# Kernel tuning notes

Measured on AMD Instinct MI355X. Metric: run time of the kernel, lower is better.

## Reference

```python
import jax, jax.numpy as jnp
import numpy as np

N_EMBED = 384
N_HEAD = 6
HEAD_DIM = N_EMBED // N_HEAD


def setup_inputs() -> dict:
    key = jax.random.key(0)
    k1, k2, k3 = jax.random.split(key, 3)
    B, T = 128, 256
    x = jax.random.normal(k1, (B, T, N_EMBED), dtype=jnp.float32)
    # nn.Linear(N_EMBED, 3*N_EMBED, bias=False): weight [3*N_EMBED, N_EMBED],
    # applied as x @ W.T -> store transposed [N_EMBED, 3*N_EMBED]
    W_qkv = jax.random.normal(k2, (N_EMBED, 3 * N_EMBED), dtype=jnp.float32) * (N_EMBED ** -0.5)
    W_proj = jax.random.normal(k3, (N_EMBED, N_EMBED), dtype=jnp.float32) * (N_EMBED ** -0.5)
    return {"x": x, "W_qkv": W_qkv, "W_proj": W_proj}


def reference(x, W_qkv, W_proj):
    B, T, C = x.shape
    qkv = jnp.einsum('btc,cd->btd', x, W_qkv)  # [B,T,3C]
    q, k, v = jnp.split(qkv, 3, axis=-1)
    # [B, H, T, Dh]
    q = q.reshape(B, T, N_HEAD, HEAD_DIM).transpose(0, 2, 1, 3)
    k = k.reshape(B, T, N_HEAD, HEAD_DIM).transpose(0, 2, 1, 3)
    v = v.reshape(B, T, N_HEAD, HEAD_DIM).transpose(0, 2, 1, 3)
    scale = HEAD_DIM ** -0.5
    wei = jnp.einsum('bhqd,bhkd->bhqk', q, k) * scale  # [B,H,T,T]
    causal = jnp.tril(jnp.ones((T, T), dtype=bool))
    wei = jnp.where(causal[None, None, :, :], wei, -jnp.inf)
    wei = jax.nn.softmax(wei, axis=-1)
    # dropout layers are identity in eval mode
    out = jnp.einsum('bhqk,bhkd->bhqd', wei, v)  # [B,H,T,Dh]
    out = out.transpose(0, 2, 1, 3).reshape(B, T, C)
    out = jnp.einsum('btc,cd->btd', out, W_proj)
    return out
```

## Files before the change

### kernel.cpp

```cpp
#include <hip/hip_runtime.h>
#include <hip/hip_bf16.h>

typedef __attribute__((ext_vector_type(8))) short short8;
typedef __attribute__((ext_vector_type(4))) float f32x4;
typedef __attribute__((ext_vector_type(4))) unsigned short ush4;

typedef const __attribute__((address_space(1))) void* gas_p;
typedef __attribute__((address_space(3))) void* las_p;
#define GLOAD_LDS16(g, l) __builtin_amdgcn_global_load_lds((gas_p)(const void*)(g), (las_p)(void*)(l), 16, 0, 0)

__device__ __forceinline__ unsigned short f2bf(float f) {
    union { float f; unsigned int u; } v; v.f = f;
    unsigned int r = v.u + 0x7FFFu + ((v.u >> 16) & 1u);
    return (unsigned short)(r >> 16);
}
__device__ __forceinline__ unsigned pk2(float a, float b) {
    return (unsigned)f2bf(a) | ((unsigned)f2bf(b) << 16);
}

__global__ __launch_bounds__(256) void cast_wt_kernel(
    const float* __restrict__ W, unsigned short* __restrict__ Wt, int K, int N)
{
    int idx = blockIdx.x * 256 + threadIdx.x;
    if (idx >= N * K) return;
    int n = idx / K, k = idx - n * K;
    Wt[idx] = f2bf(W[(size_t)k * N + n]);
}

__global__ __launch_bounds__(256, 2) void gemm_qkv_kernel(
    const float* __restrict__ x,
    const unsigned short* __restrict__ Bt,
    unsigned short* __restrict__ qkb,
    unsigned short* __restrict__ vtb)
{
    const int K = 384;
    __shared__ __align__(16) unsigned short Sh[2 * 128 * 64];
    unsigned short* As = Sh;
    unsigned short* Bs = Sh + 128 * 64;
    const int tid = threadIdx.x;
    const int lane = tid & 63, wv = tid >> 6;
    const int c = lane & 15, g = lane >> 4;
    const int wm = (wv >> 1) * 64, wn = (wv & 1) * 64;

    const int id = blockIdx.x, xcd = id & 7, kk = id >> 3;
    const long m0 = (long)(xcd * 32 + kk / 9) * 128;
    const long n0 = (long)(kk % 9) * 128;

    f32x4 acc[4][4] = {};
    const int xr = (c & 7) << 4;

    for (int kt = 0; kt < K; kt += 64) {
        #pragma unroll
        for (int i = 0; i < 4; ++i) {
            int ch = i * 256 + tid;
            int row = ch >> 3, cc = ch & 7;
            GLOAD_LDS16(&Bt[(n0 + row) * (size_t)K + kt + (cc ^ (row & 7)) * 8],
                        &Bs[(i * 256 + wv * 64) * 8]);
        }
        #pragma unroll
        for (int i = 0; i < 4; ++i) {
            int ch = i * 256 + tid;
            int row = ch >> 3, cc = ch & 7;
            const float* ga = &x[(m0 + row) * (size_t)K + kt + (cc ^ (row & 7)) * 8];
            float4 a = *(const float4*)ga;
            float4 b = *(const float4*)(ga + 4);
            uint4 w;
            w.x = pk2(a.x, a.y); w.y = pk2(a.z, a.w);
            w.z = pk2(b.x, b.y); w.w = pk2(b.z, b.w);
            *(uint4*)&As[ch * 8] = w;
        }
        __syncthreads();
        #pragma unroll
        for (int ks = 0; ks < 2; ++ks) {
            short8 af[4], bf_[4];
            #pragma unroll
            for (int i = 0; i < 4; ++i)
                af[i] = *(const short8*)((char*)As +
                    (((wm + i * 16 + c) * 128 + (ks * 32 + g * 8) * 2) ^ xr));
            #pragma unroll
            for (int i = 0; i < 4; ++i)
                bf_[i] = *(const short8*)((char*)Bs +
                    (((wn + i * 16 + c) * 128 + (ks * 32 + g * 8) * 2) ^ xr));
            #pragma unroll
            for (int mi = 0; mi < 4; ++mi)
                #pragma unroll
                for (int ni = 0; ni < 4; ++ni)
                    acc[mi][ni] = __builtin_amdgcn_mfma_f32_16x16x32_bf16(
                        af[mi], bf_[ni], acc[mi][ni], 0, 0, 0);
        }
        __syncthreads();
    }

    if (n0 < 768) {
        #pragma unroll
        for (int mi = 0; mi < 4; ++mi)
            #pragma unroll
            for (int ni = 0; ni < 4; ++ni)
                #pragma unroll
                for (int r = 0; r < 4; ++r) {
                    long m = m0 + wm + mi * 16 + g * 4 + r;
                    long n = n0 + wn + ni * 16 + c;
                    qkb[m * 768 + n] = f2bf(acc[mi][ni][r]);
                }
    } else {
        char* wbase = (char*)Sh + wv * 8192;
        #pragma unroll
        for (int ni = 0; ni < 4; ++ni)
            #pragma unroll
            for (int mi = 0; mi < 4; ++mi)
                #pragma unroll
                for (int r = 0; r < 4; ++r) {
                    int d = ni * 16 + c, t = mi * 16 + g * 4 + r;
                    int byte = (d * 128 + t * 2) ^ ((d & 7) << 4);
                    *(unsigned short*)(wbase + byte) = f2bf(acc[mi][ni][r]);
                }
        __asm__ __volatile__("" ::: "memory");
        int h = (int)((n0 + wn - 768) >> 6);
        long b = (m0 + wm) >> 8;
        int t0 = (int)((m0 + wm) & 255);
        long bh = b * 6 + h;
        #pragma unroll
        for (int it = 0; it < 8; ++it) {
            int d = it * 8 + (lane >> 3), ck = lane & 7;
            short8 v = *(const short8*)(wbase + ((d * 128 + ck * 16) ^ ((d & 7) << 4)));
            *(short8*)&vtb[(bh * 64 + d) * 256 + t0 + ck * 8] = v;
        }
    }
}

__global__ __launch_bounds__(256, 2) void gemm_proj_kernel(
    const unsigned short* __restrict__ A, const unsigned short* __restrict__ Bt,
    float* __restrict__ C, int M, int N, int K)
{
    __shared__ __align__(16) unsigned short As[128 * 64];
    __shared__ __align__(16) unsigned short Bs[128 * 64];
    const int tid = threadIdx.x;
    const int lane = tid & 63, wv = tid >> 6;
    const int c = lane & 15, g = lane >> 4;
    const int wm = (wv >> 1) * 64, wn = (wv & 1) * 64;

    const int mpx = (M >> 7) >> 3;
    const int id = blockIdx.x, xcd = id & 7, kk = id >> 3;
    const long m0 = (long)(xcd * mpx + (kk % mpx)) * 128;
    const long n0 = (long)(kk / mpx) * 128;

    f32x4 acc[4][4] = {};
    const int xr = (c & 7) << 4;

    for (int kt = 0; kt < K; kt += 64) {
        #pragma unroll
        for (int i = 0; i < 4; ++i) {
            int ch = i * 256 + wv * 64 + lane;
            int row = ch >> 3, cc = ch & 7;
            int sc = (cc ^ (row & 7)) * 8;
            GLOAD_LDS16(&A[(m0 + row) * (size_t)K + kt + sc],
                        &As[(i * 256 + wv * 64) * 8]);
            GLOAD_LDS16(&Bt[(n0 + row) * (size_t)K + kt + sc],
                        &Bs[(i * 256 + wv * 64) * 8]);
        }
        __syncthreads();
        #pragma unroll
        for (int ks = 0; ks < 2; ++ks) {
            short8 af[4], bf_[4];
            #pragma unroll
            for (int i = 0; i < 4; ++i)
                af[i] = *(const short8*)((char*)As +
                    (((wm + i * 16 + c) * 128 + (ks * 32 + g * 8) * 2) ^ xr));
            #pragma unroll
            for (int i = 0; i < 4; ++i)
                bf_[i] = *(const short8*)((char*)Bs +
                    (((wn + i * 16 + c) * 128 + (ks * 32 + g * 8) * 2) ^ xr));
            #pragma unroll
            for (int mi = 0; mi < 4; ++mi)
                #pragma unroll
                for (int ni = 0; ni < 4; ++ni)
                    acc[mi][ni] = __builtin_amdgcn_mfma_f32_16x16x32_bf16(
                        af[mi], bf_[ni], acc[mi][ni], 0, 0, 0);
        }
        __syncthreads();
    }

    #pragma unroll
    for (int mi = 0; mi < 4; ++mi)
        #pragma unroll
        for (int ni = 0; ni < 4; ++ni)
            #pragma unroll
            for (int r = 0; r < 4; ++r) {
                long m = m0 + wm + mi * 16 + g * 4 + r;
                long n = n0 + wn + ni * 16 + c;
                C[m * N + n] = acc[mi][ni][r];
            }
}

__global__ __launch_bounds__(256, 3) void attn_kernel(
    const unsigned short* __restrict__ qk,
    const unsigned short* __restrict__ vt,
    unsigned short* __restrict__ outp)
{
    const int bh = blockIdx.x;
    const int b = bh / 6, h = bh - b * 6;
    const int tid = threadIdx.x;
    const int lane = tid & 63, wv = tid >> 6;
    const int c = lane & 15, g = lane >> 4;

    __shared__ unsigned short Ks[256 * 64];
    __shared__ unsigned short Pl[4][16 * 64];

    #pragma unroll
    for (int it = 0; it < 8; ++it) {
        int ch = it * 256 + tid;
        int row = ch >> 3, col = (ch & 7) * 8;
        int db = (row * 128 + col * 2) ^ ((row & 7) << 4);
        *(short8*)((char*)Ks + db) =
            *(const short8*)&qk[(size_t)(b * 256 + row) * 768 + 384 + h * 64 + col];
    }
    __syncthreads();

    char* plw = (char*)Pl[wv];

    for (int t = 0; t < 2; ++t) {
        const int p = t ? 7 - wv : wv;
        const int jlast = p >> 1;
        const int modd = (p & 1) * 32;
        const int qt0 = p * 32;

        short8 aq[2][2];
        #pragma unroll
        for (int mi = 0; mi < 2; ++mi)
            #pragma unroll
            for (int ks = 0; ks < 2; ++ks)
                aq[mi][ks] = *(const short8*)&qk[
                    (size_t)(b * 256 + qt0 + mi * 16 + c) * 768 + h * 64 + ks * 32 + g * 8];

        f32x4 o[2][4] = {};
        float mrun[2] = {-1e30f, -1e30f}, lrun[2] = {0.f, 0.f};

        for (int j = 0; j <= jlast; ++j) {
            short8 bv[4][2];
            #pragma unroll
            for (int nd = 0; nd < 4; ++nd)
                #pragma unroll
                for (int ks = 0; ks < 2; ++ks)
                    bv[nd][ks] = *(const short8*)&vt[
                        ((size_t)bh * 64 + nd * 16 + c) * 256 + j * 64 + ks * 32 + g * 8];

            short8 bk[4][2];
            #pragma unroll
            for (int ni = 0; ni < 4; ++ni)
                #pragma unroll
                for (int ks = 0; ks < 2; ++ks) {
                    int key = j * 64 + ni * 16 + c;
                    bk[ni][ks] = *(const short8*)((char*)Ks +
                        ((key * 128 + (ks * 32 + g * 8) * 2) ^ ((key & 7) << 4)));
                }

            #pragma unroll
            for (int mi = 0; mi < 2; ++mi) {
                float pv[4][4];
                #pragma unroll
                for (int ni = 0; ni < 4; ++ni) {
                    f32x4 z = {0.f, 0.f, 0.f, 0.f};
                    z = __builtin_amdgcn_mfma_f32_16x16x32_bf16(bk[ni][0], aq[mi][0], z, 0, 0, 0);
                    z = __builtin_amdgcn_mfma_f32_16x16x32_bf16(bk[ni][1], aq[mi][1], z, 0, 0, 0);
                    #pragma unroll
                    for (int r = 0; r < 4; ++r) {
                        float v = z[r] * 0.125f;
                        if (j == jlast) {
                            int kloc = ni * 16 + g * 4 + r;
                            int qloc = mi * 16 + c + modd;
                            if (kloc > qloc) v = -1e30f;
                        }
                        pv[ni][r] = v;
                    }
                }
                float m01 = fmaxf(fmaxf(pv[0][0], pv[0][1]), fmaxf(pv[0][2], pv[0][3]));
                float m11 = fmaxf(fmaxf(pv[1][0], pv[1][1]), fmaxf(pv[1][2], pv[1][3]));
                float m21 = fmaxf(fmaxf(pv[2][0], pv[2][1]), fmaxf(pv[2][2], pv[2][3]));
                float m31 = fmaxf(fmaxf(pv[3][0], pv[3][1]), fmaxf(pv[3][2], pv[3][3]));
                float m1 = fmaxf(fmaxf(m01, m11), fmaxf(m21, m31));
                m1 = fmaxf(m1, __shfl_xor(m1, 16));
                m1 = fmaxf(m1, __shfl_xor(m1, 32));
                float mold = mrun[mi];
                float mnew = fmaxf(mold, m1);
                float fac = __expf(mold - mnew);
                float ssum = 0.f;
                #pragma unroll
                for (int ni = 0; ni < 4; ++ni)
                    #pragma unroll
                    for (int r = 0; r < 4; ++r) {
                        float pp = __expf(pv[ni][r] - mnew);
                        pv[ni][r] = pp;
                        ssum += pp;
                    }
                ssum += __shfl_xor(ssum, 16);
                ssum += __shfl_xor(ssum, 32);
                lrun[mi] = lrun[mi] * fac + ssum;
                mrun[mi] = mnew;
                #pragma unroll
                for (int nd = 0; nd < 4; ++nd)
                    #pragma unroll
                    for (int r = 0; r < 4; ++r) o[mi][nd][r] *= fac;

                __asm__ __volatile__("" ::: "memory");
                #pragma unroll
                for (int ni = 0; ni < 4; ++ni) {
                    uint2 w;
                    w.x = pk2(pv[ni][0], pv[ni][1]);
                    w.y = pk2(pv[ni][2], pv[ni][3]);
                    *(uint2*)(plw + ((c * 128 + ni * 32 + g * 8) ^ ((c & 7) << 4))) = w;
                }
                __asm__ __volatile__("" ::: "memory");

                short8 ap[2];
                #pragma unroll
                for (int ks = 0; ks < 2; ++ks)
                    ap[ks] = *(const short8*)(plw +
                        ((c * 128 + ks * 64 + g * 16) ^ ((c & 7) << 4)));

                #pragma unroll
                for (int nd = 0; nd < 4; ++nd) {
                    o[mi][nd] = __builtin_amdgcn_mfma_f32_16x16x32_bf16(bv[nd][0], ap[0], o[mi][nd], 0, 0, 0);
                    o[mi][nd] = __builtin_amdgcn_mfma_f32_16x16x32_bf16(bv[nd][1], ap[1], o[mi][nd], 0, 0, 0);
                }
                __asm__ __volatile__("" ::: "memory");
            }
        }

        #pragma unroll
        for (int mi = 0; mi < 2; ++mi) {
            float inv = 1.0f / lrun[mi];
            #pragma unroll
            for (int nd = 0; nd < 4; ++nd) {
                ush4 w;
                #pragma unroll
                for (int r = 0; r < 4; ++r) w[r] = f2bf(o[mi][nd][r] * inv);
                *(ush4*)&outp[((size_t)b * 256 + qt0 + mi * 16 + c) * 384 + h * 64 + nd * 16 + g * 4] = w;
            }
        }
    }
}

extern "C" void kernel_launch(void* const* d_in, const int* in_sizes, int n_in,
                              void* d_out, int out_size, void* d_ws, size_t ws_size,
                              hipStream_t stream) {
    const float* x     = (const float*)d_in[0];
    const float* Wqkv  = (const float*)d_in[1];
    const float* Wproj = (const float*)d_in[2];

    char* ws = (char*)d_ws;
    unsigned short* wqkvt  = (unsigned short*)(ws);
    unsigned short* wprojt = (unsigned short*)(ws + 884736);
    unsigned short* qkb    = (unsigned short*)(ws + 1179648);
    unsigned short* vtb    = (unsigned short*)(ws + 51511296);
    unsigned short* attnb  = (unsigned short*)(ws + 76677120);

    cast_wt_kernel<<<1728, 256, 0, stream>>>(Wqkv, wqkvt, 384, 1152);
    cast_wt_kernel<<<576, 256, 0, stream>>>(Wproj, wprojt, 384, 384);

    gemm_qkv_kernel<<<2304, 256, 0, stream>>>(x, wqkvt, qkb, vtb);
    attn_kernel<<<768, 256, 0, stream>>>(qkb, vtb, attnb);
    gemm_proj_kernel<<<768, 256, 0, stream>>>(attnb, wprojt, (float*)d_out, 32768, 384, 384);
}
```

Baseline: 125.1 us.

## Load fp32 x directly into LDS and convert on read; merge weight casts

The QKV GEMM now streams fp32 x into LDS with async global_load_lds and converts to bf16 during fragment reads using v_cvt_pk_bf16_f32, replacing the register-staged load, convert and LDS store. The goal is to overlap the A-tile load with the B load and remove VGPR staging. The cost is doubled A-tile LDS footprint (48KB total), which may limit occupancy. The two weight-cast launches are merged into one kernel, and the proj GEMM tile ordering puts the N tiles innermost so neighbouring blocks share A rows.

```diff
diff --git a/kernel.cpp b/kernel.cpp
--- a/kernel.cpp
+++ b/kernel.cpp
@@ -18,13 +18,20 @@
     return (unsigned)f2bf(a) | ((unsigned)f2bf(b) << 16);
 }
 
-__global__ __launch_bounds__(256) void cast_wt_kernel(
-    const float* __restrict__ W, unsigned short* __restrict__ Wt, int K, int N)
+__global__ __launch_bounds__(256) void cast_w_kernel(
+    const float* __restrict__ Wqkv, const float* __restrict__ Wproj,
+    unsigned short* __restrict__ wqkvt, unsigned short* __restrict__ wprojt)
 {
-    int idx = blockIdx.x * 256 + threadIdx.x;
-    if (idx >= N * K) return;
-    int n = idx / K, k = idx - n * K;
-    Wt[idx] = f2bf(W[(size_t)k * N + n]);
+    const int bid = blockIdx.x;
+    if (bid < 1728) {
+        int idx = bid * 256 + threadIdx.x;
+        int n = idx / 384, k = idx - n * 384;
+        wqkvt[idx] = f2bf(Wqkv[(size_t)k * 1152 + n]);
+    } else {
+        int idx = (bid - 1728) * 256 + threadIdx.x;
+        int n = idx / 384, k = idx - n * 384;
+        wprojt[idx] = f2bf(Wproj[(size_t)k * 384 + n]);
+    }
 }
 
 __global__ __launch_bounds__(256, 2) void gemm_qkv_kernel(
@@ -34,9 +41,9 @@
     unsigned short* __restrict__ vtb)
 {
     const int K = 384;
-    __shared__ __align__(16) unsigned short Sh[2 * 128 * 64];
-    unsigned short* As = Sh;
-    unsigned short* Bs = Sh + 128 * 64;
+    __shared__ __align__(16) char Sh[48 * 1024];
+    char* Af = Sh;
+    char* Bs = Sh + 32768;
     const int tid = threadIdx.x;
     const int lane = tid & 63, wv = tid >> 6;
     const int c = lane & 15, g = lane >> 4;
@@ -51,35 +58,41 @@
 
     for (int kt = 0; kt < K; kt += 64) {
         #pragma unroll
+        for (int i = 0; i < 8; ++i) {
+            int ch = i * 256 + wv * 64 + lane;
+            int row = ch >> 4, cc = ch & 15;
+            GLOAD_LDS16(&x[(m0 + row) * (size_t)K + kt + ((cc ^ (row & 7)) << 2)],
+                        Af + (i * 256 + wv * 64) * 16);
+        }
+        #pragma unroll
         for (int i = 0; i < 4; ++i) {
-            int ch = i * 256 + tid;
+            int ch = i * 256 + wv * 64 + lane;
             int row = ch >> 3, cc = ch & 7;
-            GLOAD_LDS16(&Bt[(n0 + row) * (size_t)K + kt + (cc ^ (row & 7)) * 8],
-                        &Bs[(i * 256 + wv * 64) * 8]);
-        }
-        #pragma unroll
-        for (int i = 0; i < 4; ++i) {
-            int ch = i * 256 + tid;
-            int row = ch >> 3, cc = ch & 7;
-            const float* ga = &x[(m0 + row) * (size_t)K + kt + (cc ^ (row & 7)) * 8];
-            float4 a = *(const float4*)ga;
-            float4 b = *(const float4*)(ga + 4);
-            uint4 w;
-            w.x = pk2(a.x, a.y); w.y = pk2(a.z, a.w);
-            w.z = pk2(b.x, b.y); w.w = pk2(b.z, b.w);
-            *(uint4*)&As[ch * 8] = w;
+            GLOAD_LDS16(&Bt[(n0 + row) * (size_t)K + kt + ((cc ^ (row & 7)) << 3)],
+                        Bs + (i * 256 + wv * 64) * 16);
         }
         __syncthreads();
         #pragma unroll
         for (int ks = 0; ks < 2; ++ks) {
             short8 af[4], bf_[4];
             #pragma unroll
+            for (int i = 0; i < 4; ++i) {
+                int row = wm + i * 16 + c;
+                int ch0 = ks * 8 + g * 2;
+                f32x4 lo = *(const f32x4*)(Af + row * 256 + ((ch0 ^ (c & 7)) << 4));
+                f32x4 hi = *(const f32x4*)(Af + row * 256 + (((ch0 + 1) ^ (c & 7)) << 4));
+                unsigned r0, r1, r2, r3;
+                asm("v_cvt_pk_bf16_f32 %0, %1, %2" : "=v"(r0) : "v"(lo[0]), "v"(lo[1]));
+                asm("v_cvt_pk_bf16_f32 %0, %1, %2" : "=v"(r1) : "v"(lo[2]), "v"(lo[3]));
+                asm("v_cvt_pk_bf16_f32 %0, %1, %2" : "=v"(r2) : "v"(hi[0]), "v"(hi[1]));
+                asm("v_cvt_pk_bf16_f32 %0, %1, %2" : "=v"(r3) : "v"(hi[2]), "v"(hi[3]));
+                union { uint4 u4; short8 s8; } cv;
+                cv.u4.x = r0; cv.u4.y = r1; cv.u4.z = r2; cv.u4.w = r3;
+                af[i] = cv.s8;
+            }
+            #pragma unroll
             for (int i = 0; i < 4; ++i)
-                af[i] = *(const short8*)((char*)As +
-                    (((wm + i * 16 + c) * 128 + (ks * 32 + g * 8) * 2) ^ xr));
-            #pragma unroll
-            for (int i = 0; i < 4; ++i)
-                bf_[i] = *(const short8*)((char*)Bs +
+                bf_[i] = *(const short8*)(Bs +
                     (((wn + i * 16 + c) * 128 + (ks * 32 + g * 8) * 2) ^ xr));
             #pragma unroll
             for (int mi = 0; mi < 4; ++mi)
@@ -103,7 +116,7 @@
                     qkb[m * 768 + n] = f2bf(acc[mi][ni][r]);
                 }
     } else {
-        char* wbase = (char*)Sh + wv * 8192;
+        char* wbase = Af + wv * 8192;
         #pragma unroll
         for (int ni = 0; ni < 4; ++ni)
             #pragma unroll
@@ -128,6 +141,7 @@
     }
 }
 
+template<int NP>
 __global__ __launch_bounds__(256, 2) void gemm_proj_kernel(
     const unsigned short* __restrict__ A, const unsigned short* __restrict__ Bt,
     float* __restrict__ C, int M, int N, int K)
@@ -141,8 +155,8 @@
 
     const int mpx = (M >> 7) >> 3;
     const int id = blockIdx.x, xcd = id & 7, kk = id >> 3;
-    const long m0 = (long)(xcd * mpx + (kk % mpx)) * 128;
-    const long n0 = (long)(kk / mpx) * 128;
+    const long m0 = (long)(xcd * mpx + kk / NP) * 128;
+    const long n0 = (long)(kk % NP) * 128;
 
     f32x4 acc[4][4] = {};
     const int xr = (c & 7) << 4;
@@ -354,10 +368,9 @@
     unsigned short* vtb    = (unsigned short*)(ws + 51511296);
     unsigned short* attnb  = (unsigned short*)(ws + 76677120);
 
-    cast_wt_kernel<<<1728, 256, 0, stream>>>(Wqkv, wqkvt, 384, 1152);
-    cast_wt_kernel<<<576, 256, 0, stream>>>(Wproj, wprojt, 384, 384);
+    cast_w_kernel<<<2304, 256, 0, stream>>>(Wqkv, Wproj, wqkvt, wprojt);
 
     gemm_qkv_kernel<<<2304, 256, 0, stream>>>(x, wqkvt, qkb, vtb);
     attn_kernel<<<768, 256, 0, stream>>>(qkb, vtb, attnb);
-    gemm_proj_kernel<<<768, 256, 0, stream>>>(attnb, wprojt, (float*)d_out, 32768, 384, 384);
-}
+    gemm_proj_kernel<3><<<768, 256, 0, stream>>>(attnb, wprojt, (float*)d_out, 32768, 384, 384);
+}
```

New measurement: 107.8 us. -13.8%, faster.
